# Kernel optimization log

Measured on AMD Instinct MI355X. Metric: run time of the kernel, lower is better.

The kernel has to match this reference:

```python
import jax, jax.numpy as jnp
import numpy as np

DEPTH, DIM, HEADS, DHEAD, MLP, CTX_DIM = 4, 1024, 16, 64, 4096, 1024
INNER = HEADS * DHEAD
SCALE = DHEAD ** -0.5
B, N, M = 4, 1024, 2048


def setup_inputs() -> dict:
    key = jax.random.key(0)
    ks = jax.random.split(key, 16)
    w = lambda k, shape: jax.random.normal(k, shape, dtype=jnp.float32) * 0.02
    return {
        "x": jax.random.normal(ks[0], (B, N, DIM), dtype=jnp.float32),
        "context": jax.random.normal(ks[1], (B, M, CTX_DIM), dtype=jnp.float32),
        "mask": jnp.ones((B, N), dtype=jnp.int32),
        # LayerNorm params: index 0 = pre-self-attn, 1 = pre-cross-attn, 2 = pre-FFN
        "ln_g": jnp.ones((DEPTH, 3, DIM), dtype=jnp.float32),
        "ln_b": jnp.zeros((DEPTH, 3, DIM), dtype=jnp.float32),
        "Wqkv": w(ks[2], (DEPTH, DIM, 3 * INNER)),
        "Wo_sa": w(ks[3], (DEPTH, INNER, DIM)),
        "bo_sa": jnp.zeros((DEPTH, DIM), dtype=jnp.float32),
        "Wkv": w(ks[4], (DEPTH, CTX_DIM, 2 * INNER)),
        "Wq": w(ks[5], (DEPTH, DIM, INNER)),
        "Wo_ca": w(ks[6], (DEPTH, INNER, DIM)),
        "bo_ca": jnp.zeros((DEPTH, DIM), dtype=jnp.float32),
        "W1": w(ks[7], (DEPTH, DIM, MLP)),
        "b1": jnp.zeros((DEPTH, MLP), dtype=jnp.float32),
        "W2": w(ks[8], (DEPTH, MLP, DIM)),
        "b2": jnp.zeros((DEPTH, DIM), dtype=jnp.float32),
    }


def _ln(x, g, b, eps=1e-5):
    mu = jnp.mean(x, axis=-1, keepdims=True)
    var = jnp.var(x, axis=-1, keepdims=True)
    return (x - mu) * jax.lax.rsqrt(var + eps) * g + b


def _split_heads(t):  # [b, n, h*d] -> [b, h, n, d]
    b, n, _ = t.shape
    return t.reshape(b, n, HEADS, DHEAD).transpose(0, 2, 1, 3)


def _merge_heads(t):  # [b, h, n, d] -> [b, n, h*d]
    b, h, n, d = t.shape
    return t.transpose(0, 2, 1, 3).reshape(b, n, h * d)


def _forward(x, context, mask, ln_g, ln_b, Wqkv, Wo_sa, bo_sa, Wkv, Wq, Wo_ca, bo_ca, W1, b1, W2, b2):
    neg_mask = (1 - mask).astype(x.dtype)  # [b, n]
    for i in range(DEPTH):
        # ---- self-attention (PreNorm) ----
        h = _ln(x, ln_g[i, 0], ln_b[i, 0])
        qkv = h @ Wqkv[i]
        q, k, v = jnp.split(qkv, 3, axis=-1)
        q, k, v = _split_heads(q), _split_heads(k), _split_heads(v)
        dots = jnp.einsum('bhnd,bhmd->bhnm', q, k) * SCALE
        dots = dots - neg_mask[:, None, None, :] * 1e11  # mask over keys
        attn = jax.nn.softmax(dots, axis=-1)
        out = _merge_heads(jnp.einsum('bhnm,bhmd->bhnd', attn, v))
        x = x + out @ Wo_sa[i] + bo_sa[i]
        # ---- cross-attention (PreNorm) ----
        h = _ln(x, ln_g[i, 1], ln_b[i, 1])
        kv = context @ Wkv[i]
        k, v = jnp.split(kv, 2, axis=-1)
        q = _split_heads(h @ Wq[i])
        k, v = _split_heads(k), _split_heads(v)
        dots = jnp.einsum('bhnd,bhmd->bhnm', q, k) * SCALE  # [b, h, n, m]
        dots = dots - neg_mask[:, None, :, None] * 1e6  # mask over queries
        attn = jax.nn.softmax(dots, axis=-1)
        out = _merge_heads(jnp.einsum('bhnm,bhmd->bhnd', attn, v))
        x = x + out @ Wo_ca[i] + bo_ca[i]
        # ---- feed-forward (PreNorm) ----
        h = _ln(x, ln_g[i, 2], ln_b[i, 2])
        h = jax.nn.gelu(h @ W1[i] + b1[i], approximate=False)
        x = x + h @ W2[i] + b2[i]
    return x


def reference(x, context, mask, ln_g, ln_b, Wqkv, Wo_sa, bo_sa, Wkv, Wq, Wo_ca, bo_ca, W1, b1, W2, b2):
    return _forward(x, context, mask, ln_g, ln_b, Wqkv, Wo_sa, bo_sa, Wkv, Wq, Wo_ca, bo_ca, W1, b1, W2, b2)
```

## Files before the change

kernel.cpp:

```cpp
#include <hip/hip_runtime.h>
#include <math.h>

#define DEPTH_ 4
#define DIM_ 1024
#define HEADS_ 16
#define DHEAD_ 64
#define MLP_ 4096
#define CTX_ 1024
#define INNER_ 1024
#define B_ 4
#define N_ 1024
#define M_ 2048

typedef unsigned short u16;
typedef __attribute__((ext_vector_type(4))) unsigned short u16x4;
typedef __attribute__((ext_vector_type(8))) short bf16x8;
typedef __attribute__((ext_vector_type(4))) float f32x4;
typedef __attribute__((ext_vector_type(4))) int i32x4;

#define SCQ 0.18033688011112042f

__device__ __forceinline__ u16 f2bf(float f) {
    unsigned u = __float_as_uint(f);
    return (u16)((u + 0x7fffu + ((u >> 16) & 1u)) >> 16);
}

__device__ __forceinline__ float bf2f(u16 v) {
    return __uint_as_float(((unsigned)v) << 16);
}

__device__ __forceinline__ float exp2_fast(float x) {
    float r;
    asm("v_exp_f32 %0, %1" : "=v"(r) : "v"(x));
    return r;
}

__device__ __forceinline__ float rcp_fast(float x) {
    float r;
    asm("v_rcp_f32 %0, %1" : "=v"(r) : "v"(x));
    return r;
}

__device__ __forceinline__ unsigned cvt_pk_bf16(float lo, float hi) {
    unsigned r;
    asm("v_cvt_pk_bf16_f32 %0, %1, %2" : "=v"(r) : "v"(lo), "v"(hi));
    return r;
}

__device__ __forceinline__ float gelu_fast(float v) {
    float t = v + 0.044715f * v * v * v;
    float e = exp2_fast(-2.302221673f * t);
    return v * rcp_fast(1.0f + e);
}

__device__ __forceinline__ int kv_sigma(int kv) {
    return (kv & ~31) | (((kv >> 2) & 3) << 3) | (((kv >> 4) & 1) << 2) |
           (kv & 3);
}

#define GLOAD16(gp, sp)                                                        \
    __builtin_amdgcn_global_load_lds(                                          \
        (const __attribute__((address_space(1))) void*)(gp),                   \
        (__attribute__((address_space(3))) void*)(sp), 16, 0, 0)

template <int MODE>
__global__ __launch_bounds__(256) void ln_res(
    float* __restrict__ x, const u16* __restrict__ d0,
    const u16* __restrict__ d1, const float* __restrict__ dbias,
    const float* __restrict__ g, const float* __restrict__ b,
    u16* __restrict__ y) {
    int row = blockIdx.x;
    float4 v = ((const float4*)(x + (size_t)row * DIM_))[threadIdx.x];
    if constexpr (MODE == 1) {
        u16x4 a0 = ((const u16x4*)(d0 + (size_t)row * DIM_))[threadIdx.x];
        u16x4 a1 = ((const u16x4*)(d1 + (size_t)row * DIM_))[threadIdx.x];
        float4 bb4 = ((const float4*)dbias)[threadIdx.x];
        v.x += bf2f(a0[0]) + bf2f(a1[0]) + bb4.x;
        v.y += bf2f(a0[1]) + bf2f(a1[1]) + bb4.y;
        v.z += bf2f(a0[2]) + bf2f(a1[2]) + bb4.z;
        v.w += bf2f(a0[3]) + bf2f(a1[3]) + bb4.w;
        ((float4*)(x + (size_t)row * DIM_))[threadIdx.x] = v;
    }
    float s  = v.x + v.y + v.z + v.w;
    float ss = v.x * v.x + v.y * v.y + v.z * v.z + v.w * v.w;
    #pragma unroll
    for (int off = 32; off; off >>= 1) {
        s  += __shfl_down(s, off);
        ss += __shfl_down(ss, off);
    }
    __shared__ float red[10];
    int wid = threadIdx.x >> 6, lane = threadIdx.x & 63;
    if (lane == 0) { red[wid] = s; red[4 + wid] = ss; }
    __syncthreads();
    if (threadIdx.x == 0) {
        float ts  = red[0] + red[1] + red[2] + red[3];
        float tss = red[4] + red[5] + red[6] + red[7];
        float mu  = ts * (1.0f / DIM_);
        float var = tss * (1.0f / DIM_) - mu * mu;
        red[8] = mu;
        red[9] = rsqrtf(var + 1e-5f);
    }
    __syncthreads();
    float mu = red[8], rs = red[9];
    float4 gg = ((const float4*)g)[threadIdx.x];
    float4 bb = ((const float4*)b)[threadIdx.x];
    u16x4 o;
    o[0] = f2bf((v.x - mu) * rs * gg.x + bb.x);
    o[1] = f2bf((v.y - mu) * rs * gg.y + bb.y);
    o[2] = f2bf((v.z - mu) * rs * gg.z + bb.z);
    o[3] = f2bf((v.w - mu) * rs * gg.w + bb.w);
    ((u16x4*)(y + (size_t)row * DIM_))[threadIdx.x] = o;
}

__global__ __launch_bounds__(256) void res_add(
    float* __restrict__ x, const u16* __restrict__ d0,
    const u16* __restrict__ d1, const float* __restrict__ dbias) {
    int row = blockIdx.x;
    float4 v = ((const float4*)(x + (size_t)row * DIM_))[threadIdx.x];
    u16x4 a0 = ((const u16x4*)(d0 + (size_t)row * DIM_))[threadIdx.x];
    u16x4 a1 = ((const u16x4*)(d1 + (size_t)row * DIM_))[threadIdx.x];
    float4 bb4 = ((const float4*)dbias)[threadIdx.x];
    v.x += bf2f(a0[0]) + bf2f(a1[0]) + bb4.x;
    v.y += bf2f(a0[1]) + bf2f(a1[1]) + bb4.y;
    v.z += bf2f(a0[2]) + bf2f(a1[2]) + bb4.z;
    v.w += bf2f(a0[3]) + bf2f(a1[3]) + bb4.w;
    ((float4*)(x + (size_t)row * DIM_))[threadIdx.x] = v;
}

__global__ __launch_bounds__(256) void cast_kernel(const float* __restrict__ in,
                                                   u16* __restrict__ out) {
    int i = blockIdx.x * 256 + threadIdx.x;
    float4 v = ((const float4*)in)[i];
    u16x4 o = {f2bf(v.x), f2bf(v.y), f2bf(v.z), f2bf(v.w)};
    ((u16x4*)out)[i] = o;
}

struct PrepArgs {
    const float* src[7];
    int K[7];
    int N[7];
    int dstOff[7];
    int tileCum[7];
};

__global__ __launch_bounds__(256) void prep_weights(PrepArgs a,
                                                    u16* __restrict__ wt) {
    __shared__ float tile[32][33];
    int bid = blockIdx.x;
    int wi = 0;
    while (bid >= a.tileCum[wi]) ++wi;
    int tbase = wi ? a.tileCum[wi - 1] : 0;
    int tid = bid - tbase;
    int Kd = a.K[wi], Nd = a.N[wi];
    int ntx = Nd >> 5;
    int bx = (tid % ntx) * 32;
    int by = (tid / ntx) * 32;
    const float* W = a.src[wi];
    u16* Wt = wt + a.dstOff[wi];

    int t = threadIdx.x;
    int kl = t >> 3, n4 = (t & 7) * 4;
    float4 v = *(const float4*)(W + (size_t)(by + kl) * Nd + bx + n4);
    tile[kl][n4 + 0] = v.x; tile[kl][n4 + 1] = v.y;
    tile[kl][n4 + 2] = v.z; tile[kl][n4 + 3] = v.w;
    __syncthreads();
    int nl = t >> 3, k4 = (t & 7) * 4;
    u16x4 o;
    #pragma unroll
    for (int j = 0; j < 4; ++j) o[j] = f2bf(tile[k4 + j][nl]);
    *(u16x4*)(Wt + (size_t)(bx + nl) * Kd + by + k4) = o;
}

template <int EPI, int SPLITK>
__global__ __launch_bounds__(256, 3) void gemm_mfma3(
    const u16* __restrict__ A, const u16* __restrict__ Bt,
    const float* __restrict__ bias, void* __restrict__ Cout,
    u16* __restrict__ vt, int Mdim, int Ndim, int Kdim, int nx, int ny) {
    __shared__ __align__(16) u16 As[3][128 * 32];
    __shared__ __align__(16) u16 Bs[3][128 * 32];
    const int t = threadIdx.x;
    const int lane = t & 63, w = t >> 6;
    const int c = lane & 15, g = lane >> 4;
    const int wy = w >> 1, wx = w & 1;

    const int nwg = gridDim.x;
    const int wid = (blockIdx.x & 7) * (nwg >> 3) + (blockIdx.x >> 3);
    const int bx = wid % nx;
    const int by = (wid / nx) % ny;
    const int bz = wid / (nx * ny);
    const int m0 = by * 128, n0 = bx * 128;

    f32x4 acc[4][4] = {};

    const int srow = w * 32 + (lane >> 2);
    const int scb  = (((lane & 3) ^ ((srow >> 1) & 3)) * 8);
    const u16* Ag = A + (size_t)(m0 + srow) * Kdim + scb;
    const u16* Bg = Bt + (size_t)(n0 + srow) * Kdim + scb;

    auto stage = [&](int buf, int k0) {
        GLOAD16(Ag + k0, &As[buf][w * 1024]);
        GLOAD16(Ag + k0 + (size_t)16 * Kdim, &As[buf][w * 1024 + 512]);
        GLOAD16(Bg + k0, &Bs[buf][w * 1024]);
        GLOAD16(Bg + k0 + (size_t)16 * Kdim, &Bs[buf][w * 1024 + 512]);
    };
    const int rsw = (c >> 1) & 3;
    auto compute = [&](int buf) {
        bf16x8 a[4], b[4];
        #pragma unroll
        for (int i = 0; i < 4; ++i)
            a[i] = *(const bf16x8*)&As[buf][(wy * 64 + i * 16 + c) * 32 +
                                            ((g ^ rsw) * 8)];
        #pragma unroll
        for (int j = 0; j < 4; ++j)
            b[j] = *(const bf16x8*)&Bs[buf][(wx * 64 + j * 16 + c) * 32 +
                                            ((g ^ rsw) * 8)];
        __builtin_amdgcn_s_setprio(1);
        #pragma unroll
        for (int i = 0; i < 4; ++i)
            #pragma unroll
            for (int j = 0; j < 4; ++j)
                acc[i][j] = __builtin_amdgcn_mfma_f32_16x16x32_bf16(
                    a[i], b[j], acc[i][j], 0, 0, 0);
        __builtin_amdgcn_s_setprio(0);
    };

    const int kchunk = Kdim / SPLITK;
    const int kbeg = bz * kchunk;
    const int nsteps = kchunk / 32;

    stage(0, kbeg);
    stage(1, kbeg + 32);
    int cb = 0, sb = 2;
    for (int s = 0; s < nsteps; ++s) {
        if (s + 1 < nsteps)
            asm volatile("s_waitcnt vmcnt(4)" ::: "memory");
        else
            asm volatile("s_waitcnt vmcnt(0)" ::: "memory");
        __builtin_amdgcn_s_barrier();
        if (s + 2 < nsteps) {
            stage(sb, kbeg + (s + 2) * 32);
            sb = (sb == 2) ? 0 : sb + 1;
        }
        compute(cb);
        cb = (cb == 2) ? 0 : cb + 1;
    }

    constexpr int VTHRESH = (EPI == 4) ? 2048 : 1024;
    constexpr int RPB     = (EPI == 4) ? 1024 : 2048;
    constexpr int KVL     = (EPI == 4) ? 1024 : 2048;

    const size_t outOff = (SPLITK > 1) ? (size_t)bz * Mdim * Ndim : 0;

    #pragma unroll
    for (int i = 0; i < 4; ++i) {
        int row0 = m0 + wy * 64 + i * 16 + g * 4;
        #pragma unroll
        for (int j = 0; j < 4; ++j) {
            int col = n0 + wx * 64 + j * 16 + c;
            u16x4 o4;
            #pragma unroll
            for (int r = 0; r < 4; ++r) {
                float v = acc[i][j][r];
                size_t idx = (size_t)(row0 + r) * Ndim + col;
                if constexpr (EPI == 0) {
                    ((u16*)Cout)[outOff + idx] = f2bf(v);
                } else if constexpr (EPI == 4) {
                    if (col < 1024) v *= SCQ;
                    u16 bv = f2bf(v);
                    ((u16*)Cout)[idx] = bv;
                    o4[r] = bv;
                } else if constexpr (EPI == 5) {
                    u16 bv = f2bf(v);
                    ((u16*)Cout)[idx] = bv;
                    o4[r] = bv;
                } else if constexpr (EPI == 6) {
                    ((u16*)Cout)[idx] = f2bf(v * SCQ);
                } else if constexpr (EPI == 1) {
                    v += bias[col];
                    ((u16*)Cout)[idx] = f2bf(gelu_fast(v));
                }
            }
            if constexpr (EPI == 4 || EPI == 5) {
                if (n0 + wx * 64 + j * 16 >= VTHRESH) {
                    int hh = (col - VTHRESH) >> 6;
                    int dd = col & 63;
                    int bi = row0 / RPB;
                    int kv = row0 % RPB;
                    int kvs = kv_sigma(kv);
                    *(u16x4*)&vt[(((size_t)bi * HEADS_ + hh) * 64 + dd) * KVL +
                                 kvs] = o4;
                }
            }
        }
    }
}

template <int KLEN, int IS_SA>
__global__ __launch_bounds__(256) void attn_mfma2(
    const u16* __restrict__ Qsrc, const u16* __restrict__ Ksrc,
    const u16* __restrict__ Vtg, const int* __restrict__ mask,
    u16* __restrict__ O) {
    constexpr int QSTR = IS_SA ? 3 * INNER_ : INNER_;
    constexpr int KSTR = IS_SA ? 3 * INNER_ : 2 * INNER_;
    constexpr int KOFF = IS_SA ? INNER_ : 0;

    __shared__ __align__(16) u16 Ks[2][64 * 64];
    __shared__ __align__(16) u16 Vs[2][64 * 64];

    const int t = threadIdx.x;
    const int lane = t & 63, w = t >> 6;
    const int c = lane & 15, g = lane >> 4;

    const int nwg = gridDim.x;
    const int wid = (blockIdx.x & 7) * (nwg >> 3) + (blockIdx.x >> 3);
    const int qb = wid & 15;
    const int h  = (wid >> 4) & 15;
    const int bb = wid >> 8;
    const int q0 = qb * 64;
    const int kvbase = bb * KLEN;

    const u16* qp =
        Qsrc + (size_t)(bb * N_ + q0 + w * 16 + c) * QSTR + h * 64 + g * 8;
    bf16x8 qf[2];
    qf[0] = *(const bf16x8*)qp;
    qf[1] = *(const bf16x8*)(qp + 32);

    const int sl_r = lane >> 3;
    const int scol = ((lane & 7) ^ sl_r) * 8;
    const int r0 = w * 16, r1 = w * 16 + 8;
    const u16* Kg0 = Ksrc + (size_t)(kvbase + r0 + sl_r) * KSTR + KOFF +
                     h * 64 + scol;
    const u16* Kg1 = Ksrc + (size_t)(kvbase + r1 + sl_r) * KSTR + KOFF +
                     h * 64 + scol;
    const u16* Vg0 =
        Vtg + ((size_t)(bb * HEADS_ + h) * 64 + r0 + sl_r) * KLEN + scol;
    const u16* Vg1 =
        Vtg + ((size_t)(bb * HEADS_ + h) * 64 + r1 + sl_r) * KLEN + scol;

    auto stageKV = [&](int buf, int kt) {
        GLOAD16(Kg0 + (size_t)kt * 64 * KSTR, &Ks[buf][r0 * 64]);
        GLOAD16(Kg1 + (size_t)kt * 64 * KSTR, &Ks[buf][r1 * 64]);
        GLOAD16(Vg0 + kt * 64, &Vs[buf][r0 * 64]);
        GLOAD16(Vg1 + kt * 64, &Vs[buf][r1 * 64]);
    };

    f32x4 o[4] = {};
    f32x4 lracc[4] = {};
    float mr = -1e30f;
    constexpr int NT = KLEN / 64;

    stageKV(0, 0);
    __syncthreads();
    int cur = 0;

    for (int kt = 0; kt < NT; ++kt) {
        if (kt + 1 < NT) stageKV(cur ^ 1, kt + 1);

        f32x4 sv[4] = {};
        #pragma unroll
        for (int kvb = 0; kvb < 4; ++kvb) {
            #pragma unroll
            for (int f = 0; f < 2; ++f) {
                bf16x8 kf = *(const bf16x8*)&Ks[cur][(kvb * 16 + c) * 64 +
                                                     (((g + 4 * f) ^ (c & 7)) * 8)];
                sv[kvb] = __builtin_amdgcn_mfma_f32_16x16x32_bf16(
                    kf, qf[f], sv[kvb], 0, 0, 0);
            }
        }

        if constexpr (IS_SA) {
            int mbit = mask[bb * N_ + kt * 64 + lane];
            unsigned long long ball = __ballot(mbit != 0);
            if (ball != ~0ull) {
                float negm_reg = mbit ? 0.f : 2.0e10f;
                #pragma unroll
                for (int kvb = 0; kvb < 4; ++kvb)
                    #pragma unroll
                    for (int r = 0; r < 4; ++r)
                        sv[kvb][r] -= __shfl(negm_reg, kvb * 16 + g * 4 + r);
            }
        }

        float tm = sv[0][0];
        #pragma unroll
        for (int kvb = 0; kvb < 4; ++kvb)
            #pragma unroll
            for (int r = 0; r < 4; ++r) tm = fmaxf(tm, sv[kvb][r]);

        if (!__all(tm - mr <= 8.0f)) {
            float tmc = fmaxf(tm, __shfl_xor(tm, 16));
            tmc = fmaxf(tmc, __shfl_xor(tmc, 32));
            float mn = fmaxf(mr, tmc);
            float corr = exp2_fast(mr - mn);
            mr = mn;
            #pragma unroll
            for (int kvb = 0; kvb < 4; ++kvb)
                #pragma unroll
                for (int r = 0; r < 4; ++r) lracc[kvb][r] *= corr;
            float corrO[4];
            #pragma unroll
            for (int r = 0; r < 4; ++r) corrO[r] = __shfl(corr, g * 4 + r);
            #pragma unroll
            for (int db = 0; db < 4; ++db)
                #pragma unroll
                for (int r = 0; r < 4; ++r) o[db][r] *= corrO[r];
        }

        #pragma unroll
        for (int kvb = 0; kvb < 4; ++kvb)
            #pragma unroll
            for (int r = 0; r < 4; ++r) {
                float p = exp2_fast(sv[kvb][r] - mr);
                sv[kvb][r] = p;
                lracc[kvb][r] += p;
            }

        unsigned pk[4][2];
        #pragma unroll
        for (int kvb = 0; kvb < 4; ++kvb)
            #pragma unroll
            for (int j = 0; j < 2; ++j)
                pk[kvb][j] = cvt_pk_bf16(sv[kvb][2 * j], sv[kvb][2 * j + 1]);

        #pragma unroll
        for (int pv = 0; pv < 2; ++pv) {
            i32x4 tw = {(int)pk[2 * pv][0], (int)pk[2 * pv][1],
                        (int)pk[2 * pv + 1][0], (int)pk[2 * pv + 1][1]};
            bf16x8 pa = *(bf16x8*)&tw;
            #pragma unroll
            for (int db = 0; db < 4; ++db) {
                bf16x8 vf = *(const bf16x8*)&Vs[cur][(db * 16 + c) * 64 +
                                                     (((g + 4 * pv) ^ (c & 7)) * 8)];
                o[db] = __builtin_amdgcn_mfma_f32_16x16x32_bf16(pa, vf, o[db],
                                                                0, 0, 0);
            }
        }
        __syncthreads();
        cur ^= 1;
    }

    float lr = 0.f;
    #pragma unroll
    for (int kvb = 0; kvb < 4; ++kvb)
        #pragma unroll
        for (int r = 0; r < 4; ++r) lr += lracc[kvb][r];
    lr += __shfl_xor(lr, 16);
    lr += __shfl_xor(lr, 32);

    float inv = rcp_fast(lr);
    float invO[4];
    #pragma unroll
    for (int r = 0; r < 4; ++r) invO[r] = __shfl(inv, g * 4 + r);
    #pragma unroll
    for (int db = 0; db < 4; ++db)
        #pragma unroll
        for (int r = 0; r < 4; ++r) {
            size_t idx =
                (size_t)(bb * N_ + q0 + w * 16 + g * 4 + r) * INNER_ +
                h * 64 + db * 16 + c;
            O[idx] = f2bf(o[db][r] * invO[r]);
        }
}

extern "C" void kernel_launch(void* const* d_in, const int* in_sizes, int n_in,
                              void* d_out, int out_size, void* d_ws,
                              size_t ws_size, hipStream_t stream) {
    const float* x     = (const float*)d_in[0];
    const float* ctx   = (const float*)d_in[1];
    const int*   mask  = (const int*)d_in[2];
    const float* ln_g  = (const float*)d_in[3];
    const float* ln_b  = (const float*)d_in[4];
    const float* Wqkv  = (const float*)d_in[5];
    const float* Wo_sa = (const float*)d_in[6];
    const float* bo_sa = (const float*)d_in[7];
    const float* Wkv   = (const float*)d_in[8];
    const float* Wq    = (const float*)d_in[9];
    const float* Wo_ca = (const float*)d_in[10];
    const float* bo_ca = (const float*)d_in[11];
    const float* W1    = (const float*)d_in[12];
    const float* b1    = (const float*)d_in[13];
    const float* W2    = (const float*)d_in[14];
    const float* b2    = (const float*)d_in[15];
    float* xout = (float*)d_out;

    char* ws = (char*)d_ws;
    u16* lnout = (u16*)ws;
    u16* big   = (u16*)(ws + (8ull << 20));
    u16* qca   = (u16*)(ws + (40ull << 20));
    u16* ctxb  = (u16*)(ws + (48ull << 20));
    u16* wt    = (u16*)(ws + (64ull << 20));
    u16* vt_sa = (u16*)(ws + (96ull << 20));
    u16* R1    = (u16*)(ws + (104ull << 20));
    u16* aout  = lnout;

    const int O_QKV = 0;
    const int O_WOSA = 3145728;
    const int O_WQ   = 4194304;
    const int O_WKV  = 5242880;
    const int O_WOCA = 7340032;
    const int O_W1   = 8388608;
    const int O_W2   = 12582912;

    hipMemcpyAsync(xout, x, sizeof(float) * B_ * N_ * DIM_,
                   hipMemcpyDeviceToDevice, stream);
    cast_kernel<<<B_ * M_ * CTX_ / 1024, 256, 0, stream>>>(ctx, ctxb);

    const int ROWS = B_ * N_;
    const int CROWS = B_ * M_;
    const int HALF = ROWS * DIM_;
    dim3 blk(256);

    for (int i = 0; i < DEPTH_; ++i) {
        const float* g  = ln_g + (size_t)(i * 3) * DIM_;
        const float* bb = ln_b + (size_t)(i * 3) * DIM_;

        PrepArgs pa;
        pa.src[0] = Wqkv  + (size_t)i * DIM_ * 3 * INNER_;
        pa.src[1] = Wo_sa + (size_t)i * INNER_ * DIM_;
        pa.src[2] = Wq    + (size_t)i * DIM_ * INNER_;
        pa.src[3] = Wkv   + (size_t)i * CTX_ * 2 * INNER_;
        pa.src[4] = Wo_ca + (size_t)i * INNER_ * DIM_;
        pa.src[5] = W1    + (size_t)i * DIM_ * MLP_;
        pa.src[6] = W2    + (size_t)i * MLP_ * DIM_;
        int Ks_[7] = {1024, 1024, 1024, 1024, 1024, 1024, 4096};
        int Ns_[7] = {3072, 1024, 1024, 2048, 1024, 4096, 1024};
        int Of_[7] = {O_QKV, O_WOSA, O_WQ, O_WKV, O_WOCA, O_W1, O_W2};
        int cum = 0;
        for (int k = 0; k < 7; ++k) {
            pa.K[k] = Ks_[k]; pa.N[k] = Ns_[k]; pa.dstOff[k] = Of_[k];
            cum += (Ks_[k] / 32) * (Ns_[k] / 32);
            pa.tileCum[k] = cum;
        }
        prep_weights<<<cum, blk, 0, stream>>>(pa, wt);

        if (i == 0)
            ln_res<0><<<ROWS, blk, 0, stream>>>(xout, nullptr, nullptr,
                                                nullptr, g, bb, lnout);
        else
            ln_res<1><<<ROWS, blk, 0, stream>>>(xout, R1, R1 + HALF,
                                                b2 + (size_t)(i - 1) * DIM_,
                                                g, bb, lnout);
        gemm_mfma3<4, 1><<<24 * 32, blk, 0, stream>>>(
            lnout, wt + O_QKV, nullptr, big, vt_sa, ROWS, 3 * INNER_, DIM_,
            24, 32);
        attn_mfma2<N_, 1><<<1024, blk, 0, stream>>>(big, big, vt_sa, mask,
                                                    aout);
        gemm_mfma3<0, 2><<<8 * 32 * 2, blk, 0, stream>>>(
            aout, wt + O_WOSA, nullptr, R1, nullptr, ROWS, DIM_, INNER_,
            8, 32);

        ln_res<1><<<ROWS, blk, 0, stream>>>(xout, R1, R1 + HALF,
                                            bo_sa + (size_t)i * DIM_,
                                            g + DIM_, bb + DIM_, lnout);
        gemm_mfma3<6, 1><<<8 * 32, blk, 0, stream>>>(
            lnout, wt + O_WQ, nullptr, qca, nullptr, ROWS, INNER_, DIM_,
            8, 32);
        gemm_mfma3<5, 1><<<16 * 64, blk, 0, stream>>>(
            ctxb, wt + O_WKV, nullptr, big, R1, CROWS, 2 * INNER_, CTX_,
            16, 64);
        attn_mfma2<M_, 0><<<1024, blk, 0, stream>>>(qca, big, R1, mask,
                                                    aout);
        gemm_mfma3<0, 2><<<8 * 32 * 2, blk, 0, stream>>>(
            aout, wt + O_WOCA, nullptr, R1, nullptr, ROWS, DIM_, INNER_,
            8, 32);

        ln_res<1><<<ROWS, blk, 0, stream>>>(xout, R1, R1 + HALF,
                                            bo_ca + (size_t)i * DIM_,
                                            g + 2 * DIM_, bb + 2 * DIM_,
                                            lnout);
        gemm_mfma3<1, 1><<<32 * 32, blk, 0, stream>>>(
            lnout, wt + O_W1, b1 + (size_t)i * MLP_, big, nullptr, ROWS, MLP_,
            DIM_, 32, 32);
        gemm_mfma3<0, 2><<<8 * 32 * 2, blk, 0, stream>>>(
            big, wt + O_W2, nullptr, R1, nullptr, ROWS, DIM_, MLP_, 8, 32);
    }
    res_add<<<ROWS, blk, 0, stream>>>(xout, R1, R1 + HALF,
                                      b2 + (size_t)(DEPTH_ - 1) * DIM_);
}
```

Before: 1.625 ms.

## Fuse cross-attn Q and KV GEMMs, keep residual in bf16, compute softmax sum via MFMA

```diff
diff --git a/kernel.cpp b/kernel.cpp
--- a/kernel.cpp
+++ b/kernel.cpp
@@ -41,6 +41,12 @@
     return r;
 }
 
+__device__ __forceinline__ float max3f(float a, float b, float c) {
+    float r;
+    asm("v_max3_f32 %0, %1, %2, %3" : "=v"(r) : "v"(a), "v"(b), "v"(c));
+    return r;
+}
+
 __device__ __forceinline__ unsigned cvt_pk_bf16(float lo, float hi) {
     unsigned r;
     asm("v_cvt_pk_bf16_f32 %0, %1, %2" : "=v"(r) : "v"(lo), "v"(hi));
@@ -65,12 +71,13 @@
 
 template <int MODE>
 __global__ __launch_bounds__(256) void ln_res(
-    float* __restrict__ x, const u16* __restrict__ d0,
+    u16* __restrict__ xb, const u16* __restrict__ d0,
     const u16* __restrict__ d1, const float* __restrict__ dbias,
     const float* __restrict__ g, const float* __restrict__ b,
     u16* __restrict__ y) {
     int row = blockIdx.x;
-    float4 v = ((const float4*)(x + (size_t)row * DIM_))[threadIdx.x];
+    u16x4 xv = ((const u16x4*)(xb + (size_t)row * DIM_))[threadIdx.x];
+    float4 v = {bf2f(xv[0]), bf2f(xv[1]), bf2f(xv[2]), bf2f(xv[3])};
     if constexpr (MODE == 1) {
         u16x4 a0 = ((const u16x4*)(d0 + (size_t)row * DIM_))[threadIdx.x];
         u16x4 a1 = ((const u16x4*)(d1 + (size_t)row * DIM_))[threadIdx.x];
@@ -79,7 +86,8 @@
         v.y += bf2f(a0[1]) + bf2f(a1[1]) + bb4.y;
         v.z += bf2f(a0[2]) + bf2f(a1[2]) + bb4.z;
         v.w += bf2f(a0[3]) + bf2f(a1[3]) + bb4.w;
-        ((float4*)(x + (size_t)row * DIM_))[threadIdx.x] = v;
+        u16x4 xo = {f2bf(v.x), f2bf(v.y), f2bf(v.z), f2bf(v.w)};
+        ((u16x4*)(xb + (size_t)row * DIM_))[threadIdx.x] = xo;
     }
     float s  = v.x + v.y + v.z + v.w;
     float ss = v.x * v.x + v.y * v.y + v.z * v.z + v.w * v.w;
@@ -113,18 +121,20 @@
 }
 
 __global__ __launch_bounds__(256) void res_add(
-    float* __restrict__ x, const u16* __restrict__ d0,
-    const u16* __restrict__ d1, const float* __restrict__ dbias) {
+    float* __restrict__ xout, const u16* __restrict__ xb,
+    const u16* __restrict__ d0, const u16* __restrict__ d1,
+    const float* __restrict__ dbias) {
     int row = blockIdx.x;
-    float4 v = ((const float4*)(x + (size_t)row * DIM_))[threadIdx.x];
+    u16x4 xv = ((const u16x4*)(xb + (size_t)row * DIM_))[threadIdx.x];
     u16x4 a0 = ((const u16x4*)(d0 + (size_t)row * DIM_))[threadIdx.x];
     u16x4 a1 = ((const u16x4*)(d1 + (size_t)row * DIM_))[threadIdx.x];
     float4 bb4 = ((const float4*)dbias)[threadIdx.x];
-    v.x += bf2f(a0[0]) + bf2f(a1[0]) + bb4.x;
-    v.y += bf2f(a0[1]) + bf2f(a1[1]) + bb4.y;
-    v.z += bf2f(a0[2]) + bf2f(a1[2]) + bb4.z;
-    v.w += bf2f(a0[3]) + bf2f(a1[3]) + bb4.w;
-    ((float4*)(x + (size_t)row * DIM_))[threadIdx.x] = v;
+    float4 v;
+    v.x = bf2f(xv[0]) + bf2f(a0[0]) + bf2f(a1[0]) + bb4.x;
+    v.y = bf2f(xv[1]) + bf2f(a0[1]) + bf2f(a1[1]) + bb4.y;
+    v.z = bf2f(xv[2]) + bf2f(a0[2]) + bf2f(a1[2]) + bb4.z;
+    v.w = bf2f(xv[3]) + bf2f(a0[3]) + bf2f(a1[3]) + bb4.w;
+    ((float4*)(xout + (size_t)row * DIM_))[threadIdx.x] = v;
 }
 
 __global__ __launch_bounds__(256) void cast_kernel(const float* __restrict__ in,
@@ -245,10 +255,6 @@
         cb = (cb == 2) ? 0 : cb + 1;
     }
 
-    constexpr int VTHRESH = (EPI == 4) ? 2048 : 1024;
-    constexpr int RPB     = (EPI == 4) ? 1024 : 2048;
-    constexpr int KVL     = (EPI == 4) ? 1024 : 2048;
-
     const size_t outOff = (SPLITK > 1) ? (size_t)bz * Mdim * Ndim : 0;
 
     #pragma unroll
@@ -269,27 +275,135 @@
                     u16 bv = f2bf(v);
                     ((u16*)Cout)[idx] = bv;
                     o4[r] = bv;
-                } else if constexpr (EPI == 5) {
-                    u16 bv = f2bf(v);
-                    ((u16*)Cout)[idx] = bv;
-                    o4[r] = bv;
-                } else if constexpr (EPI == 6) {
-                    ((u16*)Cout)[idx] = f2bf(v * SCQ);
                 } else if constexpr (EPI == 1) {
                     v += bias[col];
                     ((u16*)Cout)[idx] = f2bf(gelu_fast(v));
                 }
             }
-            if constexpr (EPI == 4 || EPI == 5) {
-                if (n0 + wx * 64 + j * 16 >= VTHRESH) {
-                    int hh = (col - VTHRESH) >> 6;
+            if constexpr (EPI == 4) {
+                if (n0 + wx * 64 + j * 16 >= 2048) {
+                    int hh = (col - 2048) >> 6;
                     int dd = col & 63;
-                    int bi = row0 / RPB;
-                    int kv = row0 % RPB;
+                    int bi = row0 / 1024;
+                    int kv = row0 % 1024;
                     int kvs = kv_sigma(kv);
-                    *(u16x4*)&vt[(((size_t)bi * HEADS_ + hh) * 64 + dd) * KVL +
+                    *(u16x4*)&vt[(((size_t)bi * HEADS_ + hh) * 64 + dd) * 1024 +
                                  kvs] = o4;
                 }
+            }
+        }
+    }
+}
+
+__global__ __launch_bounds__(256, 3) void gemm_dual(
+    const u16* __restrict__ Akv, const u16* __restrict__ Btkv,
+    u16* __restrict__ Ckv, u16* __restrict__ vt,
+    const u16* __restrict__ Aq, const u16* __restrict__ Btq,
+    u16* __restrict__ Cq) {
+    __shared__ __align__(16) u16 As[3][128 * 32];
+    __shared__ __align__(16) u16 Bs[3][128 * 32];
+    const int t = threadIdx.x;
+    const int lane = t & 63, w = t >> 6;
+    const int c = lane & 15, g = lane >> 4;
+    const int wy = w >> 1, wx = w & 1;
+    const int Kdim = 1024;
+
+    const int nwg = gridDim.x;
+    const int wid = (blockIdx.x & 7) * (nwg >> 3) + (blockIdx.x >> 3);
+    const bool pkv = wid < 1024;
+    const u16* A;
+    const u16* Bt;
+    u16* Cc;
+    int Ndim, bx, by;
+    if (pkv) {
+        A = Akv; Bt = Btkv; Cc = Ckv; Ndim = 2048;
+        bx = wid & 15; by = wid >> 4;
+    } else {
+        int w2 = wid - 1024;
+        A = Aq; Bt = Btq; Cc = Cq; Ndim = 1024;
+        bx = w2 & 7; by = w2 >> 3;
+    }
+    const int m0 = by * 128, n0 = bx * 128;
+
+    f32x4 acc[4][4] = {};
+
+    const int srow = w * 32 + (lane >> 2);
+    const int scb  = (((lane & 3) ^ ((srow >> 1) & 3)) * 8);
+    const u16* Ag = A + (size_t)(m0 + srow) * Kdim + scb;
+    const u16* Bg = Bt + (size_t)(n0 + srow) * Kdim + scb;
+
+    auto stage = [&](int buf, int k0) {
+        GLOAD16(Ag + k0, &As[buf][w * 1024]);
+        GLOAD16(Ag + k0 + (size_t)16 * Kdim, &As[buf][w * 1024 + 512]);
+        GLOAD16(Bg + k0, &Bs[buf][w * 1024]);
+        GLOAD16(Bg + k0 + (size_t)16 * Kdim, &Bs[buf][w * 1024 + 512]);
+    };
+    const int rsw = (c >> 1) & 3;
+    auto compute = [&](int buf) {
+        bf16x8 a[4], b[4];
+        #pragma unroll
+        for (int i = 0; i < 4; ++i)
+            a[i] = *(const bf16x8*)&As[buf][(wy * 64 + i * 16 + c) * 32 +
+                                            ((g ^ rsw) * 8)];
+        #pragma unroll
+        for (int j = 0; j < 4; ++j)
+            b[j] = *(const bf16x8*)&Bs[buf][(wx * 64 + j * 16 + c) * 32 +
+                                            ((g ^ rsw) * 8)];
+        __builtin_amdgcn_s_setprio(1);
+        #pragma unroll
+        for (int i = 0; i < 4; ++i)
+            #pragma unroll
+            for (int j = 0; j < 4; ++j)
+                acc[i][j] = __builtin_amdgcn_mfma_f32_16x16x32_bf16(
+                    a[i], b[j], acc[i][j], 0, 0, 0);
+        __builtin_amdgcn_s_setprio(0);
+    };
+
+    stage(0, 0);
+    stage(1, 32);
+    int cb = 0, sb = 2;
+    const int nsteps = 32;
+    for (int s = 0; s < nsteps; ++s) {
+        if (s + 1 < nsteps)
+            asm volatile("s_waitcnt vmcnt(4)" ::: "memory");
+        else
+            asm volatile("s_waitcnt vmcnt(0)" ::: "memory");
+        __builtin_amdgcn_s_barrier();
+        if (s + 2 < nsteps) {
+            stage(sb, (s + 2) * 32);
+            sb = (sb == 2) ? 0 : sb + 1;
+        }
+        compute(cb);
+        cb = (cb == 2) ? 0 : cb + 1;
+    }
+
+    #pragma unroll
+    for (int i = 0; i < 4; ++i) {
+        int row0 = m0 + wy * 64 + i * 16 + g * 4;
+        #pragma unroll
+        for (int j = 0; j < 4; ++j) {
+            int col = n0 + wx * 64 + j * 16 + c;
+            u16x4 o4;
+            #pragma unroll
+            for (int r = 0; r < 4; ++r) {
+                float v = acc[i][j][r];
+                size_t idx = (size_t)(row0 + r) * Ndim + col;
+                if (pkv) {
+                    u16 bv = f2bf(v);
+                    Cc[idx] = bv;
+                    o4[r] = bv;
+                } else {
+                    Cc[idx] = f2bf(v * SCQ);
+                }
+            }
+            if (pkv && (n0 + wx * 64 + j * 16 >= 1024)) {
+                int hh = (col - 1024) >> 6;
+                int dd = col & 63;
+                int bi = row0 / 2048;
+                int kv = row0 % 2048;
+                int kvs = kv_sigma(kv);
+                *(u16x4*)&vt[(((size_t)bi * HEADS_ + hh) * 64 + dd) * 2048 +
+                             kvs] = o4;
             }
         }
     }
@@ -328,33 +442,40 @@
     const int sl_r = lane >> 3;
     const int scol = ((lane & 7) ^ sl_r) * 8;
     const int r0 = w * 16, r1 = w * 16 + 8;
-    const u16* Kg0 = Ksrc + (size_t)(kvbase + r0 + sl_r) * KSTR + KOFF +
+    const u16* kp0 = Ksrc + (size_t)(kvbase + r0 + sl_r) * KSTR + KOFF +
                      h * 64 + scol;
-    const u16* Kg1 = Ksrc + (size_t)(kvbase + r1 + sl_r) * KSTR + KOFF +
+    const u16* kp1 = Ksrc + (size_t)(kvbase + r1 + sl_r) * KSTR + KOFF +
                      h * 64 + scol;
-    const u16* Vg0 =
+    const u16* vp0 =
         Vtg + ((size_t)(bb * HEADS_ + h) * 64 + r0 + sl_r) * KLEN + scol;
-    const u16* Vg1 =
+    const u16* vp1 =
         Vtg + ((size_t)(bb * HEADS_ + h) * 64 + r1 + sl_r) * KLEN + scol;
-
-    auto stageKV = [&](int buf, int kt) {
-        GLOAD16(Kg0 + (size_t)kt * 64 * KSTR, &Ks[buf][r0 * 64]);
-        GLOAD16(Kg1 + (size_t)kt * 64 * KSTR, &Ks[buf][r1 * 64]);
-        GLOAD16(Vg0 + kt * 64, &Vs[buf][r0 * 64]);
-        GLOAD16(Vg1 + kt * 64, &Vs[buf][r1 * 64]);
+    const int* mp = mask + bb * N_ + lane;
+
+    auto stageKV = [&](int buf) {
+        GLOAD16(kp0, &Ks[buf][r0 * 64]);
+        GLOAD16(kp1, &Ks[buf][r1 * 64]);
+        GLOAD16(vp0, &Vs[buf][r0 * 64]);
+        GLOAD16(vp1, &Vs[buf][r1 * 64]);
+        kp0 += (size_t)64 * KSTR;
+        kp1 += (size_t)64 * KSTR;
+        vp0 += 64;
+        vp1 += 64;
     };
 
     f32x4 o[4] = {};
-    f32x4 lracc[4] = {};
+    f32x4 oL = {};
     float mr = -1e30f;
+    const i32x4 onesI = {0x3F803F80, 0x3F803F80, 0x3F803F80, 0x3F803F80};
+    const bf16x8 ones = *(const bf16x8*)&onesI;
     constexpr int NT = KLEN / 64;
 
-    stageKV(0, 0);
+    stageKV(0);
     __syncthreads();
     int cur = 0;
 
     for (int kt = 0; kt < NT; ++kt) {
-        if (kt + 1 < NT) stageKV(cur ^ 1, kt + 1);
+        if (kt + 1 < NT) stageKV(cur ^ 1);
 
         f32x4 sv[4] = {};
         #pragma unroll
@@ -369,7 +490,8 @@
         }
 
         if constexpr (IS_SA) {
-            int mbit = mask[bb * N_ + kt * 64 + lane];
+            int mbit = *mp;
+            mp += 64;
             unsigned long long ball = __ballot(mbit != 0);
             if (ball != ~0ull) {
                 float negm_reg = mbit ? 0.f : 2.0e10f;
@@ -381,11 +503,12 @@
             }
         }
 
-        float tm = sv[0][0];
-        #pragma unroll
-        for (int kvb = 0; kvb < 4; ++kvb)
-            #pragma unroll
-            for (int r = 0; r < 4; ++r) tm = fmaxf(tm, sv[kvb][r]);
+        float x0 = max3f(sv[0][0], sv[0][1], sv[0][2]);
+        float x1 = max3f(sv[0][3], sv[1][0], sv[1][1]);
+        float x2 = max3f(sv[1][2], sv[1][3], sv[2][0]);
+        float x3 = max3f(sv[2][1], sv[2][2], sv[2][3]);
+        float x4 = max3f(sv[3][0], sv[3][1], sv[3][2]);
+        float tm = fmaxf(max3f(x0, x1, x2), max3f(x3, x4, sv[3][3]));
 
         if (!__all(tm - mr <= 8.0f)) {
             float tmc = fmaxf(tm, __shfl_xor(tm, 16));
@@ -393,10 +516,6 @@
             float mn = fmaxf(mr, tmc);
             float corr = exp2_fast(mr - mn);
             mr = mn;
-            #pragma unroll
-            for (int kvb = 0; kvb < 4; ++kvb)
-                #pragma unroll
-                for (int r = 0; r < 4; ++r) lracc[kvb][r] *= corr;
             float corrO[4];
             #pragma unroll
             for (int r = 0; r < 4; ++r) corrO[r] = __shfl(corr, g * 4 + r);
@@ -404,16 +523,15 @@
             for (int db = 0; db < 4; ++db)
                 #pragma unroll
                 for (int r = 0; r < 4; ++r) o[db][r] *= corrO[r];
+            #pragma unroll
+            for (int r = 0; r < 4; ++r) oL[r] *= corrO[r];
         }
 
         #pragma unroll
         for (int kvb = 0; kvb < 4; ++kvb)
             #pragma unroll
-            for (int r = 0; r < 4; ++r) {
-                float p = exp2_fast(sv[kvb][r] - mr);
-                sv[kvb][r] = p;
-                lracc[kvb][r] += p;
-            }
+            for (int r = 0; r < 4; ++r)
+                sv[kvb][r] = exp2_fast(sv[kvb][r] - mr);
 
         unsigned pk[4][2];
         #pragma unroll
@@ -427,6 +545,7 @@
             i32x4 tw = {(int)pk[2 * pv][0], (int)pk[2 * pv][1],
                         (int)pk[2 * pv + 1][0], (int)pk[2 * pv + 1][1]};
             bf16x8 pa = *(bf16x8*)&tw;
+            oL = __builtin_amdgcn_mfma_f32_16x16x32_bf16(pa, ones, oL, 0, 0, 0);
             #pragma unroll
             for (int db = 0; db < 4; ++db) {
                 bf16x8 vf = *(const bf16x8*)&Vs[cur][(db * 16 + c) * 64 +
@@ -439,18 +558,9 @@
         cur ^= 1;
     }
 
-    float lr = 0.f;
-    #pragma unroll
-    for (int kvb = 0; kvb < 4; ++kvb)
-        #pragma unroll
-        for (int r = 0; r < 4; ++r) lr += lracc[kvb][r];
-    lr += __shfl_xor(lr, 16);
-    lr += __shfl_xor(lr, 32);
-
-    float inv = rcp_fast(lr);
     float invO[4];
     #pragma unroll
-    for (int r = 0; r < 4; ++r) invO[r] = __shfl(inv, g * 4 + r);
+    for (int r = 0; r < 4; ++r) invO[r] = rcp_fast(oL[r]);
     #pragma unroll
     for (int db = 0; db < 4; ++db)
         #pragma unroll
@@ -489,7 +599,7 @@
     u16* qca   = (u16*)(ws + (40ull << 20));
     u16* ctxb  = (u16*)(ws + (48ull << 20));
     u16* wt    = (u16*)(ws + (64ull << 20));
-    u16* vt_sa = (u16*)(ws + (96ull << 20));
+    u16* xb    = (u16*)(ws + (96ull << 20));
     u16* R1    = (u16*)(ws + (104ull << 20));
     u16* aout  = lnout;
 
@@ -501,12 +611,10 @@
     const int O_W1   = 8388608;
     const int O_W2   = 12582912;
 
-    hipMemcpyAsync(xout, x, sizeof(float) * B_ * N_ * DIM_,
-                   hipMemcpyDeviceToDevice, stream);
     cast_kernel<<<B_ * M_ * CTX_ / 1024, 256, 0, stream>>>(ctx, ctxb);
+    cast_kernel<<<B_ * N_ * DIM_ / 1024, 256, 0, stream>>>(x, xb);
 
     const int ROWS = B_ * N_;
-    const int CROWS = B_ * M_;
     const int HALF = ROWS * DIM_;
     dim3 blk(256);
 
@@ -534,37 +642,33 @@
         prep_weights<<<cum, blk, 0, stream>>>(pa, wt);
 
         if (i == 0)
-            ln_res<0><<<ROWS, blk, 0, stream>>>(xout, nullptr, nullptr,
+            ln_res<0><<<ROWS, blk, 0, stream>>>(xb, nullptr, nullptr,
                                                 nullptr, g, bb, lnout);
         else
-            ln_res<1><<<ROWS, blk, 0, stream>>>(xout, R1, R1 + HALF,
+            ln_res<1><<<ROWS, blk, 0, stream>>>(xb, R1, R1 + HALF,
                                                 b2 + (size_t)(i - 1) * DIM_,
                                                 g, bb, lnout);
         gemm_mfma3<4, 1><<<24 * 32, blk, 0, stream>>>(
-            lnout, wt + O_QKV, nullptr, big, vt_sa, ROWS, 3 * INNER_, DIM_,
+            lnout, wt + O_QKV, nullptr, big, R1, ROWS, 3 * INNER_, DIM_,
             24, 32);
-        attn_mfma2<N_, 1><<<1024, blk, 0, stream>>>(big, big, vt_sa, mask,
+        attn_mfma2<N_, 1><<<1024, blk, 0, stream>>>(big, big, R1, mask,
                                                     aout);
         gemm_mfma3<0, 2><<<8 * 32 * 2, blk, 0, stream>>>(
             aout, wt + O_WOSA, nullptr, R1, nullptr, ROWS, DIM_, INNER_,
             8, 32);
 
-        ln_res<1><<<ROWS, blk, 0, stream>>>(xout, R1, R1 + HALF,
+        ln_res<1><<<ROWS, blk, 0, stream>>>(xb, R1, R1 + HALF,
                                             bo_sa + (size_t)i * DIM_,
                                             g + DIM_, bb + DIM_, lnout);
-        gemm_mfma3<6, 1><<<8 * 32, blk, 0, stream>>>(
-            lnout, wt + O_WQ, nullptr, qca, nullptr, ROWS, INNER_, DIM_,
-            8, 32);
-        gemm_mfma3<5, 1><<<16 * 64, blk, 0, stream>>>(
-            ctxb, wt + O_WKV, nullptr, big, R1, CROWS, 2 * INNER_, CTX_,
-            16, 64);
+        gemm_dual<<<1280, blk, 0, stream>>>(ctxb, wt + O_WKV, big, R1,
+                                            lnout, wt + O_WQ, qca);
         attn_mfma2<M_, 0><<<1024, blk, 0, stream>>>(qca, big, R1, mask,
                                                     aout);
         gemm_mfma3<0, 2><<<8 * 32 * 2, blk, 0, stream>>>(
             aout, wt + O_WOCA, nullptr, R1, nullptr, ROWS, DIM_, INNER_,
             8, 32);
 
-        ln_res<1><<<ROWS, blk, 0, stream>>>(xout, R1, R1 + HALF,
+        ln_res<1><<<ROWS, blk, 0, stream>>>(xb, R1, R1 + HALF,
                                             bo_ca + (size_t)i * DIM_,
                                             g + 2 * DIM_, bb + 2 * DIM_,
                                             lnout);
@@ -574,6 +678,6 @@
         gemm_mfma3<0, 2><<<8 * 32 * 2, blk, 0, stream>>>(
             big, wt + O_W2, nullptr, R1, nullptr, ROWS, DIM_, MLP_, 8, 32);
     }
-    res_add<<<ROWS, blk, 0, stream>>>(xout, R1, R1 + HALF,
+    res_add<<<ROWS, blk, 0, stream>>>(xout, xb, R1, R1 + HALF,
                                       b2 + (size_t)(DEPTH_ - 1) * DIM_);
 }
```

New measurement: 1.514 ms. 1.07x faster.
